# Optimization experiments

Measured on AMD Instinct MI355X. Metric: run time of the kernel, lower is better.

Reference implementation:

```python
import jax, jax.numpy as jnp
import numpy as np

N = 50000
D = 256
E = 800000


def setup_inputs() -> dict:
    key = jax.random.key(0)
    ks = jax.random.split(key, 9)
    X = jax.random.normal(ks[0], (N, D), dtype=jnp.float32)
    edge_index = jax.random.randint(ks[1], (2, E), 0, N, dtype=jnp.int32)
    edge_weight = jax.random.uniform(ks[2], (E,), dtype=jnp.float32)
    p = jax.random.normal(ks[3], (D,), dtype=jnp.float32)
    s = 1.0 / np.sqrt(D)
    W_ih = jax.random.normal(ks[4], (3 * D, D), dtype=jnp.float32) * s
    W_hh = jax.random.normal(ks[5], (3 * D, D), dtype=jnp.float32) * s
    b_ih = jax.random.normal(ks[6], (3 * D,), dtype=jnp.float32) * s
    b_hh = jax.random.normal(ks[7], (3 * D,), dtype=jnp.float32) * s
    W0 = jax.random.normal(ks[8], (D, D), dtype=jnp.float32) * s
    return {"X": X, "edge_index": edge_index, "edge_weight": edge_weight,
            "p": p, "W_ih": W_ih, "W_hh": W_hh, "b_ih": b_ih, "b_hh": b_hh, "W0": W0}


def reference(X, edge_index, edge_weight, p, W_ih, W_hh, b_ih, b_hh, W0):
    n, d = X.shape  # n=N, d=D; ratio = d/n -> TopK keeps k=d nodes
    k = d

    # ---- TopKPooling: score = X.p/||p||, keep top-k, gate by tanh(score) ----
    score = X @ p / jnp.linalg.norm(p)          # [n]
    top_score, idx = jax.lax.top_k(score, k)    # [k]
    x_tilde = X[idx] * jnp.tanh(top_score)[:, None]  # [k, d]

    # ---- Single-step GRU: input x_tilde (batch=k=d), hidden = conv weight W0 [d,d] ----
    h = W0
    gi = x_tilde @ W_ih.T + b_ih                # [d, 3d]
    gh = h @ W_hh.T + b_hh                      # [d, 3d]
    i_r, i_z, i_n = jnp.split(gi, 3, axis=1)
    h_r, h_z, h_n = jnp.split(gh, 3, axis=1)
    r = jax.nn.sigmoid(i_r + h_r)
    z = jax.nn.sigmoid(i_z + h_z)
    nn_ = jnp.tanh(i_n + r * h_n)
    W_new = (1.0 - z) * nn_ + z * h             # evolved conv weight [d, d]

    # ---- GCNConv (no bias): x = X @ W, symmetric norm with self-loops ----
    xw = X @ W_new                              # [n, d]
    src, dst = edge_index[0], edge_index[1]
    loop = jnp.arange(n, dtype=src.dtype)
    src_f = jnp.concatenate([src, loop])
    dst_f = jnp.concatenate([dst, loop])
    ew_f = jnp.concatenate([edge_weight, jnp.ones((n,), dtype=X.dtype)])
    deg = jax.ops.segment_sum(ew_f, dst_f, num_segments=n)  # [n]
    dinv = jnp.where(deg > 0, jax.lax.rsqrt(deg), 0.0)
    norm = dinv[src_f] * ew_f * dinv[dst_f]     # [E+n]
    msgs = norm[:, None] * xw[src_f]            # [E+n, d] gather
    out = jax.ops.segment_sum(msgs, dst_f, num_segments=n)  # scatter-add
    return out
```

## Files before the change

### kernel.cpp

```cpp
#include <hip/hip_runtime.h>
#include <cstdint>
#include <cstddef>

#define N_NODES 50000
#define DIM     256
#define NEDGE   800000
#define TOPK    256
#define HBINS   65536
#define CAND_CAP 2048
#define SLOT    64

typedef unsigned long long u64;
typedef float f32x4 __attribute__((ext_vector_type(4)));
typedef __bf16 b16x8 __attribute__((ext_vector_type(8)));
typedef unsigned short us8 __attribute__((ext_vector_type(8)));

__device__ __forceinline__ u64 okey(double d) {
  u64 b = (u64)__double_as_longlong(d);
  return (b & 0x8000000000000000ULL) ? ~b : (b | 0x8000000000000000ULL);
}

__device__ __forceinline__ unsigned short f2bf(float f) {
  unsigned u = __float_as_uint(f);
  return (unsigned short)((u + 0x7fffu + ((u >> 16) & 1u)) >> 16);
}

__device__ __forceinline__ float bf2f(unsigned short u) {
  return __uint_as_float(((unsigned)u) << 16);
}

__global__ void pnorm_kernel(const float* __restrict__ p, double* __restrict__ pn) {
  __shared__ double red[256];
  int t = threadIdx.x;
  double v = (double)p[t];
  red[t] = v * v;
  __syncthreads();
  for (int off = 128; off > 0; off >>= 1) {
    if (t < off) red[t] += red[t + off];
    __syncthreads();
  }
  if (t == 0) *pn = sqrt(red[0]);
}

__global__ void score_kernel(const float* __restrict__ X, const float* __restrict__ p,
                             double* __restrict__ scores, unsigned* __restrict__ hist) {
  int wid = threadIdx.x >> 6, lane = threadIdx.x & 63;
  int row = blockIdx.x * 4 + wid;
  float4 x4 = reinterpret_cast<const float4*>(X + (size_t)row * DIM)[lane];
  float4 p4 = reinterpret_cast<const float4*>(p)[lane];
  double s = (double)x4.x * p4.x + (double)x4.y * p4.y +
             (double)x4.z * p4.z + (double)x4.w * p4.w;
  for (int off = 32; off > 0; off >>= 1) s += __shfl_xor(s, off, 64);
  if (lane == 0) {
    scores[row] = s;
    unsigned bin = (unsigned)(okey(s) >> 48);
    atomicAdd(&hist[bin], 1u);
  }
}

__global__ __launch_bounds__(1024) void findbin_kernel(const unsigned* __restrict__ hist,
                                                       int* __restrict__ ctrl) {
  __shared__ int sums[1024];
  int t = threadIdx.x;
  int base = t * 64;
  const uint4* h4 = reinterpret_cast<const uint4*>(hist + base);
  int s = 0;
#pragma unroll
  for (int i = 0; i < 16; ++i) {
    uint4 v = h4[i];
    s += (int)(v.x + v.y + v.z + v.w);
  }
  sums[t] = s;
  __syncthreads();
  for (int off = 1; off < 1024; off <<= 1) {
    int x = (t + off < 1024) ? sums[t + off] : 0;
    __syncthreads();
    sums[t] += x;
    __syncthreads();
  }
  int S_incl = sums[t];
  int S_excl = S_incl - s;
  if (S_excl < TOPK && S_incl >= TOPK) {
    int c = S_excl;
    int thr = base;
    for (int b = base + 63; b >= base; --b) {
      c += (int)hist[b];
      if (c >= TOPK) { thr = b; break; }
    }
    ctrl[0] = thr;
  }
}

__global__ void collect_kernel(const double* __restrict__ scores, int* __restrict__ ctrl,
                               double* __restrict__ cand_s, int* __restrict__ cand_i) {
  int i = blockIdx.x * 256 + threadIdx.x;
  if (i >= N_NODES) return;
  double sc = scores[i];
  int bin = (int)(okey(sc) >> 48);
  if (bin >= ctrl[0]) {
    int pos = atomicAdd(&ctrl[1], 1);
    if (pos < CAND_CAP) { cand_s[pos] = sc; cand_i[pos] = i; }
  }
}

__global__ __launch_bounds__(1024) void sort_kernel(const int* __restrict__ ctrl,
                                                    const double* __restrict__ cand_s,
                                                    const int* __restrict__ cand_i,
                                                    const double* __restrict__ pn,
                                                    int* __restrict__ top_idx,
                                                    float* __restrict__ gate) {
  __shared__ double cs[CAND_CAP];
  __shared__ int ci[CAND_CAP];
  int t = threadIdx.x;
  int cnt = ctrl[1];
  if (cnt > CAND_CAP) cnt = CAND_CAP;
  for (int s = 0; s < CAND_CAP / 1024; ++s) {
    int i = t + s * 1024;
    if (i < cnt) { cs[i] = cand_s[i]; ci[i] = cand_i[i]; }
    else         { cs[i] = -1e308;    ci[i] = 0x7fffffff; }
  }
  __syncthreads();
  for (int k2 = 2; k2 <= CAND_CAP; k2 <<= 1) {
    for (int j = k2 >> 1; j > 0; j >>= 1) {
      for (int s = 0; s < CAND_CAP / 1024; ++s) {
        int i = t + s * 1024;
        int ixj = i ^ j;
        if (ixj > i) {
          double si = cs[i], sx = cs[ixj];
          int ii = ci[i], ix = ci[ixj];
          bool up = ((i & k2) == 0);
          bool sw = up ? ((sx > si) || (sx == si && ix < ii))
                       : ((si > sx) || (si == sx && ii < ix));
          if (sw) { cs[i] = sx; cs[ixj] = si; ci[i] = ix; ci[ixj] = ii; }
        }
      }
      __syncthreads();
    }
  }
  if (t < TOPK) {
    top_idx[t] = ci[t];
    gate[t] = (float)tanh(cs[t] / *pn);
  }
}

__global__ void xtilde_kernel(const float* __restrict__ X, const int* __restrict__ top_idx,
                              const float* __restrict__ gate, float* __restrict__ xt) {
  int r = blockIdx.x;
  int lane = threadIdx.x;
  float g = gate[r];
  int src = top_idx[r];
  float4 v = reinterpret_cast<const float4*>(X + (size_t)src * DIM)[lane];
  v.x *= g; v.y *= g; v.z *= g; v.w *= g;
  reinterpret_cast<float4*>(xt + (size_t)r * DIM)[lane] = v;
}

__global__ __launch_bounds__(256) void gru_gemm_kernel(const float* __restrict__ xt,
                                const float* __restrict__ W0,
                                const float* __restrict__ W_ih, const float* __restrict__ W_hh,
                                const float* __restrict__ b_ih, const float* __restrict__ b_hh,
                                float* __restrict__ gi, float* __restrict__ gh) {
  __shared__ float As[8][DIM];
  int tid = threadIdx.x;
  int c = blockIdx.x * 256 + tid;
  int r0 = blockIdx.y * 8;
  int which = blockIdx.z;
  const float* A = which ? W0 : xt;
  const float* W = which ? W_hh : W_ih;
  const float* b = which ? b_hh : b_ih;
  float* outp = which ? gh : gi;
  {
    const float4* src = reinterpret_cast<const float4*>(A + (size_t)r0 * DIM);
    float4* dst = reinterpret_cast<float4*>(&As[0][0]);
    dst[tid] = src[tid];
    dst[tid + 256] = src[tid + 256];
  }
  __syncthreads();
  const float4* Wr = reinterpret_cast<const float4*>(W + (size_t)c * DIM);
  float acc[8] = {0, 0, 0, 0, 0, 0, 0, 0};
#pragma unroll 4
  for (int k4 = 0; k4 < DIM / 4; ++k4) {
    float4 w = Wr[k4];
#pragma unroll
    for (int r = 0; r < 8; ++r) {
      acc[r] += As[r][k4 * 4 + 0] * w.x + As[r][k4 * 4 + 1] * w.y +
                As[r][k4 * 4 + 2] * w.z + As[r][k4 * 4 + 3] * w.w;
    }
  }
  float bc = b[c];
#pragma unroll
  for (int r = 0; r < 8; ++r)
    outp[(size_t)(r0 + r) * 768 + c] = acc[r] + bc;
}

__global__ void wnew_kernel(const float* __restrict__ gi, const float* __restrict__ gh,
                            const float* __restrict__ W0, unsigned short* __restrict__ Wnbt) {
  int rr = blockIdx.x, c = threadIdx.x;
  const float* gir = gi + (size_t)rr * 768;
  const float* ghr = gh + (size_t)rr * 768;
  float i_r = gir[c],       h_r = ghr[c];
  float i_z = gir[c + 256], h_z = ghr[c + 256];
  float i_n = gir[c + 512], h_n = ghr[c + 512];
  float r = 1.f / (1.f + expf(-(i_r + h_r)));
  float z = 1.f / (1.f + expf(-(i_z + h_z)));
  float nn = tanhf(i_n + r * h_n);
  float h = W0[(size_t)rr * DIM + c];
  float w = (1.f - z) * nn + z * h;
  Wnbt[(size_t)c * DIM + rr] = f2bf(w);
}

__global__ __launch_bounds__(256) void xw_mfma_kernel(const float* __restrict__ X,
                                                      const unsigned short* __restrict__ Wnbt,
                                                      unsigned short* __restrict__ xwb) {
  int wid = threadIdx.x >> 6, lane = threadIdx.x & 63;
  int r0 = blockIdx.x * 64 + wid * 16;
  if (r0 >= N_NODES) return;
  int rowA = r0 + (lane & 15);
  int kgrp = lane >> 4;
  int koff = kgrp * 8;

  const float4* Ar = reinterpret_cast<const float4*>(X + (size_t)rowA * DIM);
  b16x8 afr[8];
#pragma unroll
  for (int kt = 0; kt < 8; ++kt) {
    float4 f0 = Ar[kt * 8 + kgrp * 2 + 0];
    float4 f1 = Ar[kt * 8 + kgrp * 2 + 1];
    union { us8 u; b16x8 b; } cv;
    cv.u[0] = f2bf(f0.x); cv.u[1] = f2bf(f0.y); cv.u[2] = f2bf(f0.z); cv.u[3] = f2bf(f0.w);
    cv.u[4] = f2bf(f1.x); cv.u[5] = f2bf(f1.y); cv.u[6] = f2bf(f1.z); cv.u[7] = f2bf(f1.w);
    afr[kt] = cv.b;
  }

  int colB = lane & 15;
  const unsigned short* Bbase = Wnbt + (size_t)colB * DIM + koff;
  int rr = r0 + kgrp * 4;
#pragma unroll 4
  for (int nf = 0; nf < 16; ++nf) {
    f32x4 acc = {0.f, 0.f, 0.f, 0.f};
    const unsigned short* Bp = Bbase + (size_t)nf * 16 * DIM;
#pragma unroll
    for (int kt = 0; kt < 8; ++kt) {
      b16x8 bfr = *reinterpret_cast<const b16x8*>(Bp + kt * 32);
      acc = __builtin_amdgcn_mfma_f32_16x16x32_bf16(afr[kt], bfr, acc, 0, 0, 0);
    }
    int cc = nf * 16 + colB;
#pragma unroll
    for (int j = 0; j < 4; ++j)
      xwb[(size_t)(rr + j) * DIM + cc] = f2bf(acc[j]);
  }
}

__global__ void edeg_kernel(const int* __restrict__ ei, const float* __restrict__ ew,
                            float* __restrict__ deg) {
  int e = blockIdx.x * 256 + threadIdx.x;
  if (e >= NEDGE) return;
  int d = ei[NEDGE + e];
  atomicAdd(&deg[d], ew[e]);
}

__global__ void scatter_kernel(const int* __restrict__ ei, const float* __restrict__ ew,
                               const float* __restrict__ deg,
                               int* __restrict__ fill, u64* __restrict__ colval) {
  int e = blockIdx.x * 256 + threadIdx.x;
  if (e >= NEDGE) return;
  int s = ei[e], d = ei[NEDGE + e];
  float v = ew[e] * __frsqrt_rn(deg[s] + 1.0f);
  int pos = atomicAdd(&fill[d], 1);
  if (pos < SLOT)
    colval[(size_t)d * SLOT + pos] = ((u64)__float_as_uint(v) << 32) | (unsigned)s;
}

__global__ __launch_bounds__(256) void agg_kernel(const unsigned short* __restrict__ xwb,
                           const float* __restrict__ deg,
                           const int* __restrict__ fill, const u64* __restrict__ colval,
                           float* __restrict__ out) {
  int wid = threadIdx.x >> 6, lane = threadIdx.x & 63;
  int i = blockIdx.x * 4 + wid;
  float di = __frsqrt_rn(deg[i] + 1.0f);
  ushort4 sv = reinterpret_cast<const ushort4*>(xwb + (size_t)i * DIM)[lane];
  float4 acc;
  acc.x = di * bf2f(sv.x); acc.y = di * bf2f(sv.y);
  acc.z = di * bf2f(sv.z); acc.w = di * bf2f(sv.w);
  int n = fill[i];
  if (n > SLOT) n = SLOT;
  const u64* cv = colval + (size_t)i * SLOT;
  int j = 0;
  for (; j + 4 <= n; j += 4) {
    u64 a0 = cv[j], a1 = cv[j + 1], a2 = cv[j + 2], a3 = cv[j + 3];
    ushort4 m0 = reinterpret_cast<const ushort4*>(xwb + (size_t)(unsigned)a0 * DIM)[lane];
    ushort4 m1 = reinterpret_cast<const ushort4*>(xwb + (size_t)(unsigned)a1 * DIM)[lane];
    ushort4 m2 = reinterpret_cast<const ushort4*>(xwb + (size_t)(unsigned)a2 * DIM)[lane];
    ushort4 m3 = reinterpret_cast<const ushort4*>(xwb + (size_t)(unsigned)a3 * DIM)[lane];
    float v0 = __uint_as_float((unsigned)(a0 >> 32));
    float v1 = __uint_as_float((unsigned)(a1 >> 32));
    float v2 = __uint_as_float((unsigned)(a2 >> 32));
    float v3 = __uint_as_float((unsigned)(a3 >> 32));
    acc.x += v0 * bf2f(m0.x); acc.y += v0 * bf2f(m0.y);
    acc.z += v0 * bf2f(m0.z); acc.w += v0 * bf2f(m0.w);
    acc.x += v1 * bf2f(m1.x); acc.y += v1 * bf2f(m1.y);
    acc.z += v1 * bf2f(m1.z); acc.w += v1 * bf2f(m1.w);
    acc.x += v2 * bf2f(m2.x); acc.y += v2 * bf2f(m2.y);
    acc.z += v2 * bf2f(m2.z); acc.w += v2 * bf2f(m2.w);
    acc.x += v3 * bf2f(m3.x); acc.y += v3 * bf2f(m3.y);
    acc.z += v3 * bf2f(m3.z); acc.w += v3 * bf2f(m3.w);
  }
  for (; j < n; ++j) {
    u64 a0 = cv[j];
    ushort4 m0 = reinterpret_cast<const ushort4*>(xwb + (size_t)(unsigned)a0 * DIM)[lane];
    float v0 = __uint_as_float((unsigned)(a0 >> 32));
    acc.x += v0 * bf2f(m0.x); acc.y += v0 * bf2f(m0.y);
    acc.z += v0 * bf2f(m0.z); acc.w += v0 * bf2f(m0.w);
  }
  acc.x *= di; acc.y *= di; acc.z *= di; acc.w *= di;
  reinterpret_cast<float4*>(out + (size_t)i * DIM)[lane] = acc;
}

extern "C" void kernel_launch(void* const* d_in, const int* in_sizes, int n_in,
                              void* d_out, int out_size, void* d_ws, size_t ws_size,
                              hipStream_t stream) {
  const float* X    = (const float*)d_in[0];
  const int*   ei   = (const int*)d_in[1];
  const float* ew   = (const float*)d_in[2];
  const float* p    = (const float*)d_in[3];
  const float* W_ih = (const float*)d_in[4];
  const float* W_hh = (const float*)d_in[5];
  const float* b_ih = (const float*)d_in[6];
  const float* b_hh = (const float*)d_in[7];
  const float* W0   = (const float*)d_in[8];
  float* out = (float*)d_out;

  char* ws = (char*)d_ws;
  size_t off = 0;
  auto alloc = [&](size_t bytes) { size_t o = off; off = (off + bytes + 255) & ~(size_t)255; return o; };

  size_t hist_o  = alloc(HBINS * 4);
  size_t ctrl_o  = alloc(64);
  size_t deg_o   = alloc(N_NODES * 4);
  size_t fill_o  = alloc(N_NODES * 4);
  size_t zero_span = off;
  size_t scores_o = alloc(N_NODES * 8);
  size_t pn_o     = alloc(8);
  size_t cands_o  = alloc(CAND_CAP * 8);
  size_t candi_o  = alloc(CAND_CAP * 4);
  size_t topidx_o = alloc(TOPK * 4);
  size_t gate_o   = alloc(TOPK * 4);
  size_t xt_o     = alloc((size_t)TOPK * DIM * 4);
  size_t gi_o     = alloc((size_t)256 * 768 * 4);
  size_t gh_o     = alloc((size_t)256 * 768 * 4);
  size_t wnbt_o   = alloc((size_t)DIM * DIM * 2);
  size_t colval_o = alloc((size_t)N_NODES * SLOT * 8);
  size_t xwb_o    = alloc((size_t)N_NODES * DIM * 2);
  (void)ws_size; (void)n_in; (void)in_sizes; (void)out_size;

  unsigned* hist  = (unsigned*)(ws + hist_o);
  int*    ctrl    = (int*)(ws + ctrl_o);
  float*  deg     = (float*)(ws + deg_o);
  int*    fill    = (int*)(ws + fill_o);
  double* scores  = (double*)(ws + scores_o);
  double* pn      = (double*)(ws + pn_o);
  double* cand_s  = (double*)(ws + cands_o);
  int*    cand_i  = (int*)(ws + candi_o);
  int*    top_idx = (int*)(ws + topidx_o);
  float*  gate    = (float*)(ws + gate_o);
  float*  xt      = (float*)(ws + xt_o);
  float*  gi      = (float*)(ws + gi_o);
  float*  gh      = (float*)(ws + gh_o);
  unsigned short* Wnbt = (unsigned short*)(ws + wnbt_o);
  u64*    colval  = (u64*)(ws + colval_o);
  unsigned short* xwb = (unsigned short*)(ws + xwb_o);

  hipMemsetAsync(ws, 0, zero_span, stream);

  pnorm_kernel<<<1, 256, 0, stream>>>(p, pn);
  score_kernel<<<N_NODES / 4, 256, 0, stream>>>(X, p, scores, hist);
  findbin_kernel<<<1, 1024, 0, stream>>>(hist, ctrl);
  collect_kernel<<<(N_NODES + 255) / 256, 256, 0, stream>>>(scores, ctrl, cand_s, cand_i);
  sort_kernel<<<1, 1024, 0, stream>>>(ctrl, cand_s, cand_i, pn, top_idx, gate);
  xtilde_kernel<<<TOPK, 64, 0, stream>>>(X, top_idx, gate, xt);
  gru_gemm_kernel<<<dim3(3, 32, 2), 256, 0, stream>>>(xt, W0, W_ih, W_hh, b_ih, b_hh, gi, gh);
  wnew_kernel<<<256, 256, 0, stream>>>(gi, gh, W0, Wnbt);
  xw_mfma_kernel<<<(N_NODES + 63) / 64, 256, 0, stream>>>(X, Wnbt, xwb);
  edeg_kernel<<<(NEDGE + 255) / 256, 256, 0, stream>>>(ei, ew, deg);
  scatter_kernel<<<(NEDGE + 255) / 256, 256, 0, stream>>>(ei, ew, deg, fill, colval);
  agg_kernel<<<N_NODES / 4, 256, 0, stream>>>(xwb, deg, fill, colval, out);
}
```

Before: 520.4 us.

## Fuse degree and CSR scatter, precompute dinv, use grid-stride loops

```diff
diff --git a/kernel.cpp b/kernel.cpp
--- a/kernel.cpp
+++ b/kernel.cpp
@@ -42,19 +42,23 @@
   if (t == 0) *pn = sqrt(red[0]);
 }
 
-__global__ void score_kernel(const float* __restrict__ X, const float* __restrict__ p,
+__global__ __launch_bounds__(256) void score_kernel(const float* __restrict__ X,
+                             const float* __restrict__ p,
                              double* __restrict__ scores, unsigned* __restrict__ hist) {
-  int wid = threadIdx.x >> 6, lane = threadIdx.x & 63;
-  int row = blockIdx.x * 4 + wid;
-  float4 x4 = reinterpret_cast<const float4*>(X + (size_t)row * DIM)[lane];
+  int lane = threadIdx.x & 63;
+  int gw = blockIdx.x * 4 + (threadIdx.x >> 6);
+  int nw = gridDim.x * 4;
   float4 p4 = reinterpret_cast<const float4*>(p)[lane];
-  double s = (double)x4.x * p4.x + (double)x4.y * p4.y +
-             (double)x4.z * p4.z + (double)x4.w * p4.w;
-  for (int off = 32; off > 0; off >>= 1) s += __shfl_xor(s, off, 64);
-  if (lane == 0) {
-    scores[row] = s;
-    unsigned bin = (unsigned)(okey(s) >> 48);
-    atomicAdd(&hist[bin], 1u);
+  for (int row = gw; row < N_NODES; row += nw) {
+    float4 x4 = reinterpret_cast<const float4*>(X + (size_t)row * DIM)[lane];
+    double s = (double)x4.x * p4.x + (double)x4.y * p4.y +
+               (double)x4.z * p4.z + (double)x4.w * p4.w;
+    for (int off = 32; off > 0; off >>= 1) s += __shfl_xor(s, off, 64);
+    if (lane == 0) {
+      scores[row] = s;
+      unsigned bin = (unsigned)(okey(s) >> 48);
+      atomicAdd(&hist[bin], 1u);
+    }
   }
 }
 
@@ -249,69 +253,75 @@
   }
 }
 
-__global__ void edeg_kernel(const int* __restrict__ ei, const float* __restrict__ ew,
-                            float* __restrict__ deg) {
-  int e = blockIdx.x * 256 + threadIdx.x;
-  if (e >= NEDGE) return;
-  int d = ei[NEDGE + e];
-  atomicAdd(&deg[d], ew[e]);
-}
-
-__global__ void scatter_kernel(const int* __restrict__ ei, const float* __restrict__ ew,
-                               const float* __restrict__ deg,
+__global__ __launch_bounds__(256) void scatter_kernel(const int* __restrict__ ei,
+                               const float* __restrict__ ew,
+                               float* __restrict__ deg,
                                int* __restrict__ fill, u64* __restrict__ colval) {
-  int e = blockIdx.x * 256 + threadIdx.x;
-  if (e >= NEDGE) return;
-  int s = ei[e], d = ei[NEDGE + e];
-  float v = ew[e] * __frsqrt_rn(deg[s] + 1.0f);
-  int pos = atomicAdd(&fill[d], 1);
-  if (pos < SLOT)
-    colval[(size_t)d * SLOT + pos] = ((u64)__float_as_uint(v) << 32) | (unsigned)s;
+  int stride = gridDim.x * 256;
+  for (int e = blockIdx.x * 256 + threadIdx.x; e < NEDGE; e += stride) {
+    int s = ei[e], d = ei[NEDGE + e];
+    float w = ew[e];
+    atomicAdd(&deg[d], w);
+    int pos = atomicAdd(&fill[d], 1);
+    if (pos < SLOT)
+      colval[(size_t)d * SLOT + pos] = ((u64)__float_as_uint(w) << 32) | (unsigned)s;
+  }
+}
+
+__global__ void dinv_kernel(const float* __restrict__ deg, float* __restrict__ dinvb) {
+  int i = blockIdx.x * 256 + threadIdx.x;
+  if (i >= N_NODES) return;
+  dinvb[i] = __frsqrt_rn(deg[i] + 1.0f);
 }
 
 __global__ __launch_bounds__(256) void agg_kernel(const unsigned short* __restrict__ xwb,
-                           const float* __restrict__ deg,
+                           const float* __restrict__ dinvb,
                            const int* __restrict__ fill, const u64* __restrict__ colval,
                            float* __restrict__ out) {
-  int wid = threadIdx.x >> 6, lane = threadIdx.x & 63;
-  int i = blockIdx.x * 4 + wid;
-  float di = __frsqrt_rn(deg[i] + 1.0f);
-  ushort4 sv = reinterpret_cast<const ushort4*>(xwb + (size_t)i * DIM)[lane];
-  float4 acc;
-  acc.x = di * bf2f(sv.x); acc.y = di * bf2f(sv.y);
-  acc.z = di * bf2f(sv.z); acc.w = di * bf2f(sv.w);
-  int n = fill[i];
-  if (n > SLOT) n = SLOT;
-  const u64* cv = colval + (size_t)i * SLOT;
-  int j = 0;
-  for (; j + 4 <= n; j += 4) {
-    u64 a0 = cv[j], a1 = cv[j + 1], a2 = cv[j + 2], a3 = cv[j + 3];
-    ushort4 m0 = reinterpret_cast<const ushort4*>(xwb + (size_t)(unsigned)a0 * DIM)[lane];
-    ushort4 m1 = reinterpret_cast<const ushort4*>(xwb + (size_t)(unsigned)a1 * DIM)[lane];
-    ushort4 m2 = reinterpret_cast<const ushort4*>(xwb + (size_t)(unsigned)a2 * DIM)[lane];
-    ushort4 m3 = reinterpret_cast<const ushort4*>(xwb + (size_t)(unsigned)a3 * DIM)[lane];
-    float v0 = __uint_as_float((unsigned)(a0 >> 32));
-    float v1 = __uint_as_float((unsigned)(a1 >> 32));
-    float v2 = __uint_as_float((unsigned)(a2 >> 32));
-    float v3 = __uint_as_float((unsigned)(a3 >> 32));
-    acc.x += v0 * bf2f(m0.x); acc.y += v0 * bf2f(m0.y);
-    acc.z += v0 * bf2f(m0.z); acc.w += v0 * bf2f(m0.w);
-    acc.x += v1 * bf2f(m1.x); acc.y += v1 * bf2f(m1.y);
-    acc.z += v1 * bf2f(m1.z); acc.w += v1 * bf2f(m1.w);
-    acc.x += v2 * bf2f(m2.x); acc.y += v2 * bf2f(m2.y);
-    acc.z += v2 * bf2f(m2.z); acc.w += v2 * bf2f(m2.w);
-    acc.x += v3 * bf2f(m3.x); acc.y += v3 * bf2f(m3.y);
-    acc.z += v3 * bf2f(m3.z); acc.w += v3 * bf2f(m3.w);
-  }
-  for (; j < n; ++j) {
-    u64 a0 = cv[j];
-    ushort4 m0 = reinterpret_cast<const ushort4*>(xwb + (size_t)(unsigned)a0 * DIM)[lane];
-    float v0 = __uint_as_float((unsigned)(a0 >> 32));
-    acc.x += v0 * bf2f(m0.x); acc.y += v0 * bf2f(m0.y);
-    acc.z += v0 * bf2f(m0.z); acc.w += v0 * bf2f(m0.w);
-  }
-  acc.x *= di; acc.y *= di; acc.z *= di; acc.w *= di;
-  reinterpret_cast<float4*>(out + (size_t)i * DIM)[lane] = acc;
+  int lane = threadIdx.x & 63;
+  int gw = blockIdx.x * 4 + (threadIdx.x >> 6);
+  int nw = gridDim.x * 4;
+  for (int i = gw; i < N_NODES; i += nw) {
+    float di = dinvb[i];
+    ushort4 sv = reinterpret_cast<const ushort4*>(xwb + (size_t)i * DIM)[lane];
+    float4 acc;
+    acc.x = di * bf2f(sv.x); acc.y = di * bf2f(sv.y);
+    acc.z = di * bf2f(sv.z); acc.w = di * bf2f(sv.w);
+    int n = fill[i];
+    if (n > SLOT) n = SLOT;
+    const u64* cv = colval + (size_t)i * SLOT;
+    int j = 0;
+    for (; j + 4 <= n; j += 4) {
+      u64 a0 = cv[j], a1 = cv[j + 1], a2 = cv[j + 2], a3 = cv[j + 3];
+      unsigned c0 = (unsigned)a0, c1 = (unsigned)a1, c2 = (unsigned)a2, c3 = (unsigned)a3;
+      ushort4 m0 = reinterpret_cast<const ushort4*>(xwb + (size_t)c0 * DIM)[lane];
+      ushort4 m1 = reinterpret_cast<const ushort4*>(xwb + (size_t)c1 * DIM)[lane];
+      ushort4 m2 = reinterpret_cast<const ushort4*>(xwb + (size_t)c2 * DIM)[lane];
+      ushort4 m3 = reinterpret_cast<const ushort4*>(xwb + (size_t)c3 * DIM)[lane];
+      float v0 = __uint_as_float((unsigned)(a0 >> 32)) * dinvb[c0];
+      float v1 = __uint_as_float((unsigned)(a1 >> 32)) * dinvb[c1];
+      float v2 = __uint_as_float((unsigned)(a2 >> 32)) * dinvb[c2];
+      float v3 = __uint_as_float((unsigned)(a3 >> 32)) * dinvb[c3];
+      acc.x += v0 * bf2f(m0.x); acc.y += v0 * bf2f(m0.y);
+      acc.z += v0 * bf2f(m0.z); acc.w += v0 * bf2f(m0.w);
+      acc.x += v1 * bf2f(m1.x); acc.y += v1 * bf2f(m1.y);
+      acc.z += v1 * bf2f(m1.z); acc.w += v1 * bf2f(m1.w);
+      acc.x += v2 * bf2f(m2.x); acc.y += v2 * bf2f(m2.y);
+      acc.z += v2 * bf2f(m2.z); acc.w += v2 * bf2f(m2.w);
+      acc.x += v3 * bf2f(m3.x); acc.y += v3 * bf2f(m3.y);
+      acc.z += v3 * bf2f(m3.z); acc.w += v3 * bf2f(m3.w);
+    }
+    for (; j < n; ++j) {
+      u64 a0 = cv[j];
+      unsigned c0 = (unsigned)a0;
+      ushort4 m0 = reinterpret_cast<const ushort4*>(xwb + (size_t)c0 * DIM)[lane];
+      float v0 = __uint_as_float((unsigned)(a0 >> 32)) * dinvb[c0];
+      acc.x += v0 * bf2f(m0.x); acc.y += v0 * bf2f(m0.y);
+      acc.z += v0 * bf2f(m0.z); acc.w += v0 * bf2f(m0.w);
+    }
+    acc.x *= di; acc.y *= di; acc.z *= di; acc.w *= di;
+    reinterpret_cast<float4*>(out + (size_t)i * DIM)[lane] = acc;
+  }
 }
 
 extern "C" void kernel_launch(void* const* d_in, const int* in_sizes, int n_in,
@@ -343,6 +353,7 @@
   size_t candi_o  = alloc(CAND_CAP * 4);
   size_t topidx_o = alloc(TOPK * 4);
   size_t gate_o   = alloc(TOPK * 4);
+  size_t dinv_o   = alloc(N_NODES * 4);
   size_t xt_o     = alloc((size_t)TOPK * DIM * 4);
   size_t gi_o     = alloc((size_t)256 * 768 * 4);
   size_t gh_o     = alloc((size_t)256 * 768 * 4);
@@ -361,6 +372,7 @@
   int*    cand_i  = (int*)(ws + candi_o);
   int*    top_idx = (int*)(ws + topidx_o);
   float*  gate    = (float*)(ws + gate_o);
+  float*  dinvb   = (float*)(ws + dinv_o);
   float*  xt      = (float*)(ws + xt_o);
   float*  gi      = (float*)(ws + gi_o);
   float*  gh      = (float*)(ws + gh_o);
@@ -371,7 +383,7 @@
   hipMemsetAsync(ws, 0, zero_span, stream);
 
   pnorm_kernel<<<1, 256, 0, stream>>>(p, pn);
-  score_kernel<<<N_NODES / 4, 256, 0, stream>>>(X, p, scores, hist);
+  score_kernel<<<1024, 256, 0, stream>>>(X, p, scores, hist);
   findbin_kernel<<<1, 1024, 0, stream>>>(hist, ctrl);
   collect_kernel<<<(N_NODES + 255) / 256, 256, 0, stream>>>(scores, ctrl, cand_s, cand_i);
   sort_kernel<<<1, 1024, 0, stream>>>(ctrl, cand_s, cand_i, pn, top_idx, gate);
@@ -379,7 +391,7 @@
   gru_gemm_kernel<<<dim3(3, 32, 2), 256, 0, stream>>>(xt, W0, W_ih, W_hh, b_ih, b_hh, gi, gh);
   wnew_kernel<<<256, 256, 0, stream>>>(gi, gh, W0, Wnbt);
   xw_mfma_kernel<<<(N_NODES + 63) / 64, 256, 0, stream>>>(X, Wnbt, xwb);
-  edeg_kernel<<<(NEDGE + 255) / 256, 256, 0, stream>>>(ei, ew, deg);
-  scatter_kernel<<<(NEDGE + 255) / 256, 256, 0, stream>>>(ei, ew, deg, fill, colval);
-  agg_kernel<<<N_NODES / 4, 256, 0, stream>>>(xwb, deg, fill, colval, out);
-}
+  scatter_kernel<<<1024, 256, 0, stream>>>(ei, ew, deg, fill, colval);
+  dinv_kernel<<<(N_NODES + 255) / 256, 256, 0, stream>>>(deg, dinvb);
+  agg_kernel<<<2048, 256, 0, stream>>>(xwb, dinvb, fill, colval, out);
+}
```

After: 529.5 us. About the same (+1.7%).
